# Optimization experiments

Hardware: AMD Instinct MI355X
Metric: run time of the kernel (lower is better)

The kernel has to match this reference:

```python
import jax, jax.numpy as jnp
import numpy as np

B, W, F, H = 2048, 128, 8, 256
LN_EPS = 1e-5


def _gru_cell(h, xt, Wih, Whh, bih, bhh):
    # PyTorch GRU cell. Wih: [3H, Fin], Whh: [3H, H]
    gi = xt @ Wih.T + bih            # [B, 3H]
    gh = h @ Whh.T + bhh             # [B, 3H]
    ir, iz, inn = jnp.split(gi, 3, axis=-1)
    hr, hz, hn = jnp.split(gh, 3, axis=-1)
    r = jax.nn.sigmoid(ir + hr)
    z = jax.nn.sigmoid(iz + hz)
    n = jnp.tanh(inn + r * hn)
    return (1.0 - z) * n + z * h


def setup_inputs() -> dict:
    key = jax.random.key(0)
    ks = jax.random.split(key, 12)
    s = 1.0 / np.sqrt(H)   # torch GRU init: U(-1/sqrt(H), 1/sqrt(H))
    sp = 1.0 / np.sqrt(2 * H)  # torch Linear init fan_in = 2H
    u = lambda k, shp, sc: jax.random.uniform(k, shp, jnp.float32, -sc, sc)
    return {
        "x": jax.random.normal(ks[0], (B, W, F), jnp.float32),
        "Wih_f": u(ks[1], (3 * H, F), s), "Whh_f": u(ks[2], (3 * H, H), s),
        "bih_f": u(ks[3], (3 * H,), s), "bhh_f": u(ks[4], (3 * H,), s),
        "Wih_b": u(ks[5], (3 * H, F), s), "Whh_b": u(ks[6], (3 * H, H), s),
        "bih_b": u(ks[7], (3 * H,), s), "bhh_b": u(ks[8], (3 * H,), s),
        "Wp": u(ks[9], (H, 2 * H), sp), "bp": u(ks[10], (H,), sp),
        "gamma": jnp.ones((H,), jnp.float32), "beta": jnp.zeros((H,), jnp.float32),
    }


def reference(x, Wih_f, Whh_f, bih_f, bhh_f, Wih_b, Whh_b, bih_b, bhh_b, Wp, bp, gamma, beta):
    b = x.shape[0]
    h0 = jnp.zeros((b, H), x.dtype)
    xs = jnp.swapaxes(x, 0, 1)  # [W, B, F]
    # Forward direction: only the final hidden state is used (out[:, -1, :H]).
    h_fwd, _ = jax.lax.scan(
        lambda h, xt: (_gru_cell(h, xt, Wih_f, Whh_f, bih_f, bhh_f), None), h0, xs)
    # Backward direction output at the LAST time index is its FIRST step
    # (reversed scan starting from h0 on x[:, -1]).
    h_bwd = _gru_cell(h0, x[:, -1, :], Wih_b, Whh_b, bih_b, bhh_b)
    last = jnp.concatenate([h_fwd, h_bwd], axis=-1)  # [B, 2H]
    y = jax.nn.gelu(last @ Wp.T + bp, approximate=False)
    mu = jnp.mean(y, axis=-1, keepdims=True)
    var = jnp.var(y, axis=-1, keepdims=True)
    yn = (y - mu) * jax.lax.rsqrt(var + LN_EPS)
    return yn * gamma + beta  # dropout is identity in eval mode
```

## Files before the change

### kernel.cpp

```cpp
#include <hip/hip_runtime.h>
#include <hip/hip_bf16.h>

#define BDIM 2048
#define WDIM 128
#define FDIM 8
#define HDIM 256

typedef __bf16 b8 __attribute__((ext_vector_type(8)));
typedef __bf16 b4 __attribute__((ext_vector_type(4)));
typedef float f32x4 __attribute__((ext_vector_type(4)));

#define OFF_RZ  0
#define OFF_N   262144
#define OFF_WIH 393216
#define OFF_WP  442368
#define OFF_XB  704512

#define SMEM_BYTES 147456

#define MFMA(a,b,c) __builtin_amdgcn_mfma_f32_16x16x32_bf16((a),(b),(c),0,0,0)

static __device__ __forceinline__ float sig_(float v) {
    return __builtin_amdgcn_rcpf(1.0f + __expf(-v));
}
static __device__ __forceinline__ float tanh_(float v) {
    return fmaf(-2.0f, __builtin_amdgcn_rcpf(1.0f + __expf(2.0f * v)), 1.0f);
}

__global__ void pack_kernel(const float* __restrict__ x,
                            const float* __restrict__ Wih_f,
                            const float* __restrict__ Whh_f,
                            const float* __restrict__ bih_f,
                            const float* __restrict__ bhh_f,
                            const float* __restrict__ Wp,
                            unsigned char* __restrict__ ws)
{
    int idx = blockIdx.x * 256 + threadIdx.x;
    if (idx < 16384) {
        int l = idx & 63, f = idx >> 6;
        int kt = f & 7, nt = (f >> 3) & 1, g = (f >> 4) & 1, w = f >> 5;
        int gch = g * HDIM + 32 * w + 16 * nt + (l & 15);
        int kb = kt * 32 + (l >> 4) * 8;
        b8 v;
        #pragma unroll
        for (int e = 0; e < 8; ++e) v[e] = (__bf16)Whh_f[gch * HDIM + kb + e];
        ((b8*)(ws + OFF_RZ))[idx] = v;
    } else if (idx < 24576) {
        int j = idx - 16384;
        int l = j & 63, f = j >> 6;
        int kt = f & 7, nt = (f >> 3) & 1, w = f >> 4;
        int gch = 2 * HDIM + 32 * w + 16 * nt + (l & 15);
        int kb = kt * 32 + (l >> 4) * 8;
        b8 v;
        #pragma unroll
        for (int e = 0; e < 8; ++e) v[e] = (__bf16)Whh_f[gch * HDIM + kb + e];
        ((b8*)(ws + OFF_N))[j] = v;
    } else if (idx < 27648) {
        int j = idx - 24576;
        int l = j & 63, f = j >> 6;
        int nt = f & 1, q = f >> 1, g = q % 3, w = q / 3;
        int gch = g * HDIM + 32 * w + 16 * nt + (l & 15);
        int lq = l >> 4;
        b8 v;
        #pragma unroll
        for (int e = 0; e < 8; ++e) v[e] = (__bf16)0.0f;
        if (lq == 0) {
            #pragma unroll
            for (int e = 0; e < 8; ++e) v[e] = (__bf16)Wih_f[gch * FDIM + e];
        } else if (lq == 1) {
            float b = (g == 2) ? bih_f[gch] : (bih_f[gch] + bhh_f[gch]);
            v[0] = (__bf16)b;
        }
        ((b8*)(ws + OFF_WIH))[j] = v;
    } else if (idx < 44032) {
        int j = idx - 27648;
        int l = j & 63, nk = j >> 6;
        int NT = nk >> 4, kt = nk & 15;
        int col = NT * 16 + (l & 15);
        int kb = kt * 32 + (l >> 4) * 8;
        b8 v;
        #pragma unroll
        for (int e = 0; e < 8; ++e) v[e] = (__bf16)Wp[col * (2 * HDIM) + kb + e];
        ((b8*)(ws + OFF_WP))[j] = v;
    } else if (idx < 44032 + 262144) {
        int j = idx - 44032;
        const float* src = x + j * 8;
        b8 v;
        #pragma unroll
        for (int e = 0; e < 8; ++e) v[e] = (__bf16)src[e];
        ((b8*)(ws + OFF_XB))[j] = v;
    }
}

__global__ __launch_bounds__(512, 2)
void gru_main_kernel(const float* __restrict__ x,
                     const float* __restrict__ bhh_f,
                     const float* __restrict__ Wih_b, const float* __restrict__ bih_b,
                     const float* __restrict__ bhh_b,
                     const float* __restrict__ bp,
                     const float* __restrict__ gamma, const float* __restrict__ beta,
                     const unsigned char* __restrict__ ws,
                     float* __restrict__ out)
{
    extern __shared__ __align__(16) unsigned char smem[];
    __bf16* hbB = (__bf16*)smem;
    b8* nlds = (b8*)(smem + 16384);
    __bf16 (*lastb)[2 * HDIM] = (__bf16(*)[2 * HDIM])smem;
    float  (*ybuf)[HDIM]      = (float(*)[HDIM])(smem + 16384);

    const int tid = threadIdx.x, lane = tid & 63, w = tid >> 6;
    const int l15 = lane & 15, lq = lane >> 4;
    const int blockRow = blockIdx.x * 16;

    const b8* wsRZ = (const b8*)(ws + OFF_RZ);
    const b8* wsN  = (const b8*)(ws + OFF_N);
    const b8* wsWI = (const b8*)(ws + OFF_WIH);
    const b8* wsWP = (const b8*)(ws + OFF_WP);
    const b8* xB   = (const b8*)(ws + OFF_XB);

    const f32x4 zero4 = {0.f, 0.f, 0.f, 0.f};

    *(f32x4*)(smem + tid * 16) = zero4;
    *(f32x4*)(smem + 8192 + tid * 16) = zero4;

    {
        const b8* nsrc = wsN + (w * 16) * 64 + lane;
        b8* ndst = nlds + (w * 16) * 64 + lane;
        #pragma unroll
        for (int i = 0; i < 16; ++i) ndst[i * 64] = nsrc[i * 64];
    }

    b8 whr[2][8], whz[2][8], wir[2], wiz[2], win[2];
    #pragma unroll
    for (int nt = 0; nt < 2; ++nt) {
        #pragma unroll
        for (int kt = 0; kt < 8; ++kt) {
            whr[nt][kt] = wsRZ[((w * 4 + 0 + nt) * 8 + kt) * 64 + lane];
            whz[nt][kt] = wsRZ[((w * 4 + 2 + nt) * 8 + kt) * 64 + lane];
        }
        wir[nt] = wsWI[((w * 3 + 0) * 2 + nt) * 64 + lane];
        wiz[nt] = wsWI[((w * 3 + 1) * 2 + nt) * 64 + lane];
        win[nt] = wsWI[((w * 3 + 2) * 2 + nt) * 64 + lane];
    }
    #pragma unroll
    for (int nt = 0; nt < 2; ++nt) {
        #pragma unroll
        for (int kt = 0; kt < 8; ++kt) {
            asm volatile("" : "+v"(whr[nt][kt]));
            asm volatile("" : "+v"(whz[nt][kt]));
        }
        asm volatile("" : "+v"(wir[nt]));
        asm volatile("" : "+v"(wiz[nt]));
        asm volatile("" : "+v"(win[nt]));
    }

    const float4 bnv0 = *(const float4*)&bhh_f[2 * HDIM + 32 * w + 0  + 4 * lq];
    const float4 bnv1 = *(const float4*)&bhh_f[2 * HDIM + 32 * w + 16 + 4 * lq];

    b8 xc;
    #pragma unroll
    for (int e = 0; e < 8; ++e) xc[e] = (__bf16)0.0f;
    if (lq == 1) xc[0] = (__bf16)1.0f;

    f32x4 h0 = zero4, h1 = zero4;

    const int kswz = (8 * lq) ^ ((l15 & 7) << 3);
    const int wswz = (l15 & 7) << 3;
    const b8* nW = nlds + (w * 16) * 64 + lane;
    const b8* xRow = xB + (blockRow + l15) * WDIM;

    b8 xf = xc;
    if (lane < 16) xf = xRow[0];

    __syncthreads();

    int cur = 0;
    for (int t = 0; t < WDIM; ++t) {
        b8 xn = xc;
        if (lane < 16) xn = xRow[(t < WDIM - 1) ? (t + 1) : t];

        const __bf16* hc = hbB + cur * 4096 + l15 * 256;

        f32x4 aR0 = zero4, aR1 = zero4;
        f32x4 aZ0 = zero4, aZ1 = zero4;
        f32x4 aNH0, aNH1;
        aNH0[0] = bnv0.x; aNH0[1] = bnv0.y; aNH0[2] = bnv0.z; aNH0[3] = bnv0.w;
        aNH1[0] = bnv1.x; aNH1[1] = bnv1.y; aNH1[2] = bnv1.z; aNH1[3] = bnv1.w;

        #pragma unroll
        for (int kt = 0; kt < 8; ++kt) {
            b8 hfrag = *(const b8*)(hc + ((kt << 5) ^ kswz));
            b8 n0 = nW[kt * 64];
            b8 n1 = nW[(8 + kt) * 64];
            aR0  = MFMA(whr[0][kt], hfrag, aR0);
            aR1  = MFMA(whr[1][kt], hfrag, aR1);
            aZ0  = MFMA(whz[0][kt], hfrag, aZ0);
            aZ1  = MFMA(whz[1][kt], hfrag, aZ1);
            aNH0 = MFMA(n0, hfrag, aNH0);
            aNH1 = MFMA(n1, hfrag, aNH1);
        }
        aR0 = MFMA(wir[0], xf, aR0);
        aR1 = MFMA(wir[1], xf, aR1);
        aZ0 = MFMA(wiz[0], xf, aZ0);
        aZ1 = MFMA(wiz[1], xf, aZ1);
        f32x4 aNX0 = MFMA(win[0], xf, zero4);
        f32x4 aNX1 = MFMA(win[1], xf, zero4);

        __bf16* hn = hbB + (cur ^ 1) * 4096;
        b4 v0, v1;
        #pragma unroll
        for (int j = 0; j < 4; ++j) {
            float r = sig_(aR0[j]);
            float z = sig_(aZ0[j]);
            float n = tanh_(fmaf(r, aNH0[j], aNX0[j]));
            float hv = n + z * (h0[j] - n);
            h0[j] = hv; v0[j] = (__bf16)hv;
            r = sig_(aR1[j]);
            z = sig_(aZ1[j]);
            n = tanh_(fmaf(r, aNH1[j], aNX1[j]));
            hv = n + z * (h1[j] - n);
            h1[j] = hv; v1[j] = (__bf16)hv;
        }
        *(b4*)(hn + l15 * 256 + ((32 * w + 0  + 4 * lq) ^ wswz)) = v0;
        *(b4*)(hn + l15 * 256 + ((32 * w + 16 + 4 * lq) ^ wswz)) = v1;

        xf = xn;
        cur ^= 1;
        __syncthreads();
    }

    {
        b4 v0, v1;
        #pragma unroll
        for (int j = 0; j < 4; ++j) { v0[j] = (__bf16)h0[j]; v1[j] = (__bf16)h1[j]; }
        *(b4*)(&lastb[l15][0] + ((32 * w + 0  + 4 * lq) ^ wswz)) = v0;
        *(b4*)(&lastb[l15][0] + ((32 * w + 16 + 4 * lq) ^ wswz)) = v1;
    }

    {
        const int trow = tid >> 5;
        const int cb = tid & 31;
        const float4* xr = (const float4*)(x + (blockRow + trow) * WDIM * FDIM + 127 * FDIM);
        float4 xv0 = xr[0], xv1 = xr[1];
        const float4* wb = (const float4*)Wih_b;
        #pragma unroll
        for (int jj = 0; jj < 8; ++jj) {
            int ch = cb + 32 * jj;
            float4 a0 = wb[ch * 2],              a1 = wb[ch * 2 + 1];
            float4 b0 = wb[(HDIM + ch) * 2],     b1 = wb[(HDIM + ch) * 2 + 1];
            float4 c0 = wb[(2 * HDIM + ch) * 2], c1 = wb[(2 * HDIM + ch) * 2 + 1];
            float ir = bih_b[ch]
                + xv0.x * a0.x + xv0.y * a0.y + xv0.z * a0.z + xv0.w * a0.w
                + xv1.x * a1.x + xv1.y * a1.y + xv1.z * a1.z + xv1.w * a1.w;
            float iz = bih_b[HDIM + ch]
                + xv0.x * b0.x + xv0.y * b0.y + xv0.z * b0.z + xv0.w * b0.w
                + xv1.x * b1.x + xv1.y * b1.y + xv1.z * b1.z + xv1.w * b1.w;
            float inn = bih_b[2 * HDIM + ch]
                + xv0.x * c0.x + xv0.y * c0.y + xv0.z * c0.z + xv0.w * c0.w
                + xv1.x * c1.x + xv1.y * c1.y + xv1.z * c1.z + xv1.w * c1.w;
            float r = sig_(ir + bhh_b[ch]);
            float z = sig_(iz + bhh_b[HDIM + ch]);
            float n = tanh_(fmaf(r, bhh_b[2 * HDIM + ch], inn));
            float hbw = (1.0f - z) * n;
            int c2 = HDIM + ch;
            lastb[trow][c2 ^ ((trow & 7) << 3)] = (__bf16)hbw;
        }
    }
    __syncthreads();

    {
        f32x4 pacc[2];
        #pragma unroll
        for (int nt = 0; nt < 2; ++nt) {
            int col = 32 * w + nt * 16 + l15;
            float b = bp[col];
            pacc[nt][0] = b; pacc[nt][1] = b; pacc[nt][2] = b; pacc[nt][3] = b;
        }
        #pragma unroll
        for (int kt = 0; kt < 16; ++kt) {
            int c = (kt * 32 + lq * 8) ^ ((l15 & 7) << 3);
            b8 a = *(const b8*)&lastb[l15][c];
            #pragma unroll
            for (int nt = 0; nt < 2; ++nt)
                pacc[nt] = MFMA(a, wsWP[((2 * w + nt) * 16 + kt) * 64 + lane], pacc[nt]);
        }
        #pragma unroll
        for (int nt = 0; nt < 2; ++nt) {
            int col = 32 * w + nt * 16 + l15;
            #pragma unroll
            for (int j = 0; j < 4; ++j) {
                int row = lq * 4 + j;
                float v = pacc[nt][j];
                ybuf[row][col] = 0.5f * v * (1.0f + erff(v * 0.70710678118f));
            }
        }
    }
    __syncthreads();

    #pragma unroll
    for (int rr = 0; rr < 2; ++rr) {
        int row = 2 * w + rr;
        float v[4];
        float s = 0.0f, sq = 0.0f;
        #pragma unroll
        for (int m = 0; m < 4; ++m) {
            v[m] = ybuf[row][lane + 64 * m];
            s += v[m];
            sq += v[m] * v[m];
        }
        #pragma unroll
        for (int off = 32; off >= 1; off >>= 1) {
            s  += __shfl_xor(s, off, 64);
            sq += __shfl_xor(sq, off, 64);
        }
        float mu = s * (1.0f / 256.0f);
        float var = sq * (1.0f / 256.0f) - mu * mu;
        float rs = rsqrtf(var + 1e-5f);
        float* orow = out + (blockRow + row) * HDIM;
        #pragma unroll
        for (int m = 0; m < 4; ++m) {
            int cc = lane + 64 * m;
            orow[cc] = (v[m] - mu) * rs * gamma[cc] + beta[cc];
        }
    }
}

extern "C" void kernel_launch(void* const* d_in, const int* in_sizes, int n_in,
                              void* d_out, int out_size, void* d_ws, size_t ws_size,
                              hipStream_t stream)
{
    const float* x     = (const float*)d_in[0];
    const float* Wih_f = (const float*)d_in[1];
    const float* Whh_f = (const float*)d_in[2];
    const float* bih_f = (const float*)d_in[3];
    const float* bhh_f = (const float*)d_in[4];
    const float* Wih_b = (const float*)d_in[5];
    const float* bih_b = (const float*)d_in[7];
    const float* bhh_b = (const float*)d_in[8];
    const float* Wp    = (const float*)d_in[9];
    const float* bp    = (const float*)d_in[10];
    const float* gamma = (const float*)d_in[11];
    const float* beta  = (const float*)d_in[12];
    float* out = (float*)d_out;
    unsigned char* ws = (unsigned char*)d_ws;

    hipFuncSetAttribute((const void*)gru_main_kernel,
                        hipFuncAttributeMaxDynamicSharedMemorySize, SMEM_BYTES);

    const int packItems = 16384 + 8192 + 3072 + 16384 + 262144;
    hipLaunchKernelGGL(pack_kernel, dim3((packItems + 255) / 256), dim3(256), 0, stream,
                       x, Wih_f, Whh_f, bih_f, bhh_f, Wp, ws);
    hipLaunchKernelGGL(gru_main_kernel, dim3(BDIM / 16), dim3(512), SMEM_BYTES, stream,
                       x, bhh_f, Wih_b, bih_b, bhh_b, bp, gamma, beta, ws, out);
}
```

Measured before the change: 216.0 us.

## Keep all recurrent GRU weights in registers and stage input weights in LDS

```diff
diff --git a/kernel.cpp b/kernel.cpp
--- a/kernel.cpp
+++ b/kernel.cpp
@@ -16,7 +16,7 @@
 #define OFF_WP  442368
 #define OFF_XB  704512
 
-#define SMEM_BYTES 147456
+#define SMEM_BYTES 65536
 
 #define MFMA(a,b,c) __builtin_amdgcn_mfma_f32_16x16x32_bf16((a),(b),(c),0,0,0)
 
@@ -104,7 +104,7 @@
 {
     extern __shared__ __align__(16) unsigned char smem[];
     __bf16* hbB = (__bf16*)smem;
-    b8* nlds = (b8*)(smem + 16384);
+    b8* wihL = (b8*)(smem + 16384);
     __bf16 (*lastb)[2 * HDIM] = (__bf16(*)[2 * HDIM])smem;
     float  (*ybuf)[HDIM]      = (float(*)[HDIM])(smem + 16384);
 
@@ -124,23 +124,21 @@
     *(f32x4*)(smem + 8192 + tid * 16) = zero4;
 
     {
-        const b8* nsrc = wsN + (w * 16) * 64 + lane;
-        b8* ndst = nlds + (w * 16) * 64 + lane;
-        #pragma unroll
-        for (int i = 0; i < 16; ++i) ndst[i * 64] = nsrc[i * 64];
-    }
-
-    b8 whr[2][8], whz[2][8], wir[2], wiz[2], win[2];
+        const b8* src = wsWI + (w * 6) * 64 + lane;
+        b8* dst = wihL + (w * 6) * 64 + lane;
+        #pragma unroll
+        for (int i = 0; i < 6; ++i) dst[i * 64] = src[i * 64];
+    }
+
+    b8 whr[2][8], whz[2][8], wnn[2][8];
     #pragma unroll
     for (int nt = 0; nt < 2; ++nt) {
         #pragma unroll
         for (int kt = 0; kt < 8; ++kt) {
             whr[nt][kt] = wsRZ[((w * 4 + 0 + nt) * 8 + kt) * 64 + lane];
             whz[nt][kt] = wsRZ[((w * 4 + 2 + nt) * 8 + kt) * 64 + lane];
-        }
-        wir[nt] = wsWI[((w * 3 + 0) * 2 + nt) * 64 + lane];
-        wiz[nt] = wsWI[((w * 3 + 1) * 2 + nt) * 64 + lane];
-        win[nt] = wsWI[((w * 3 + 2) * 2 + nt) * 64 + lane];
+            wnn[nt][kt] = wsN[((w * 2 + nt) * 8 + kt) * 64 + lane];
+        }
     }
     #pragma unroll
     for (int nt = 0; nt < 2; ++nt) {
@@ -148,10 +146,8 @@
         for (int kt = 0; kt < 8; ++kt) {
             asm volatile("" : "+v"(whr[nt][kt]));
             asm volatile("" : "+v"(whz[nt][kt]));
-        }
-        asm volatile("" : "+v"(wir[nt]));
-        asm volatile("" : "+v"(wiz[nt]));
-        asm volatile("" : "+v"(win[nt]));
+            asm volatile("" : "+v"(wnn[nt][kt]));
+        }
     }
 
     const float4 bnv0 = *(const float4*)&bhh_f[2 * HDIM + 32 * w + 0  + 4 * lq];
@@ -166,7 +162,7 @@
 
     const int kswz = (8 * lq) ^ ((l15 & 7) << 3);
     const int wswz = (l15 & 7) << 3;
-    const b8* nW = nlds + (w * 16) * 64 + lane;
+    const b8* wihB = wihL + (w * 6) * 64 + lane;
     const b8* xRow = xB + (blockRow + l15) * WDIM;
 
     b8 xf = xc;
@@ -177,34 +173,34 @@
     int cur = 0;
     for (int t = 0; t < WDIM; ++t) {
         b8 xn = xc;
-        if (lane < 16) xn = xRow[(t < WDIM - 1) ? (t + 1) : t];
-
-        const __bf16* hc = hbB + cur * 4096 + l15 * 256;
-
-        f32x4 aR0 = zero4, aR1 = zero4;
-        f32x4 aZ0 = zero4, aZ1 = zero4;
+        if (lane < 16) xn = xRow[(t + 1) & 127];
+
+        b8 wfr0 = wihB[0 * 64], wfr1 = wihB[1 * 64];
+        b8 wfz0 = wihB[2 * 64], wfz1 = wihB[3 * 64];
+        b8 wfn0 = wihB[4 * 64], wfn1 = wihB[5 * 64];
+
+        f32x4 aR0 = MFMA(wfr0, xf, zero4);
+        f32x4 aR1 = MFMA(wfr1, xf, zero4);
+        f32x4 aZ0 = MFMA(wfz0, xf, zero4);
+        f32x4 aZ1 = MFMA(wfz1, xf, zero4);
+        f32x4 aNX0 = MFMA(wfn0, xf, zero4);
+        f32x4 aNX1 = MFMA(wfn1, xf, zero4);
+
         f32x4 aNH0, aNH1;
         aNH0[0] = bnv0.x; aNH0[1] = bnv0.y; aNH0[2] = bnv0.z; aNH0[3] = bnv0.w;
         aNH1[0] = bnv1.x; aNH1[1] = bnv1.y; aNH1[2] = bnv1.z; aNH1[3] = bnv1.w;
 
+        const __bf16* hc = hbB + cur * 4096 + l15 * 256;
         #pragma unroll
         for (int kt = 0; kt < 8; ++kt) {
             b8 hfrag = *(const b8*)(hc + ((kt << 5) ^ kswz));
-            b8 n0 = nW[kt * 64];
-            b8 n1 = nW[(8 + kt) * 64];
             aR0  = MFMA(whr[0][kt], hfrag, aR0);
             aR1  = MFMA(whr[1][kt], hfrag, aR1);
             aZ0  = MFMA(whz[0][kt], hfrag, aZ0);
             aZ1  = MFMA(whz[1][kt], hfrag, aZ1);
-            aNH0 = MFMA(n0, hfrag, aNH0);
-            aNH1 = MFMA(n1, hfrag, aNH1);
-        }
-        aR0 = MFMA(wir[0], xf, aR0);
-        aR1 = MFMA(wir[1], xf, aR1);
-        aZ0 = MFMA(wiz[0], xf, aZ0);
-        aZ1 = MFMA(wiz[1], xf, aZ1);
-        f32x4 aNX0 = MFMA(win[0], xf, zero4);
-        f32x4 aNX1 = MFMA(win[1], xf, zero4);
+            aNH0 = MFMA(wnn[0][kt], hfrag, aNH0);
+            aNH1 = MFMA(wnn[1][kt], hfrag, aNH1);
+        }
 
         __bf16* hn = hbB + (cur ^ 1) * 4096;
         b4 v0, v1;
```

After: 309.2 us. 43.1% more time.
